# Optimization experiments

Hardware: AMD Instinct MI355X
Metric: run time of the kernel (lower is better)

Reference implementation:

```python
import jax, jax.numpy as jnp
import numpy as np

B, S, D = 4, 4096, 256


def setup_inputs() -> dict:
    key = jax.random.key(0)
    ks = jax.random.split(key, 12)
    s = 0.05
    return {
        "v": jax.random.normal(ks[0], (B, S, D), jnp.float32),
        "k": jax.random.normal(ks[1], (B, S, D), jnp.float32),
        "q": jax.random.normal(ks[2], (B, S, D), jnp.float32),
        "mask": jax.random.uniform(ks[3], (B, S, S), jnp.float32),
        "wq_k": jax.random.normal(ks[4], (D, D), jnp.float32) * s,
        "wq_b": jnp.zeros((D,), jnp.float32),
        "wk_k": jax.random.normal(ks[5], (D, D), jnp.float32) * s,
        "wk_b": jnp.zeros((D,), jnp.float32),
        "wv_k": jax.random.normal(ks[6], (D, D), jnp.float32) * s,
        "wv_b": jnp.zeros((D,), jnp.float32),
        "anchor": jax.random.normal(ks[7], (S, D), jnp.float32) * s,
        "dense_k": jax.random.normal(ks[8], (D, D), jnp.float32) * s,
        "dense_b": jnp.zeros((D,), jnp.float32),
    }


def reference(v, k, q, mask, wq_k, wq_b, wk_k, wk_b, wv_k, wv_b, anchor, dense_k, dense_b):
    # Bipolar linear projections
    qp = q @ wq_k + wq_b  # [B,Sq,D]
    kp = k @ wk_k + wk_b  # [B,Sk,D]
    vp = v @ wv_k + wv_b  # [B,Sk,D]

    # else-branch (Sq != D): k_ext = sign(k)[:,:,None,:] + sign(q)[:,None,:,:]
    # logits[b,i,j] = sum_d (sign(k)+sign(q))*sign(q)
    #              = sign(k)@sign(q)^T + sum_d sign(q)^2  (exact factorization)
    sq = jnp.sign(qp)
    sk = jnp.sign(kp)
    logits = (jnp.einsum('bkd,bqd->bkq', sk, sq)
              + jnp.sum(sq * sq, axis=-1)[:, None, :]) / 1024.0  # [B,Sk,Sq]

    attn = jax.nn.softmax(logits, axis=-1)  # softmax over Sq
    attn = attn * mask                      # mask applied AFTER softmax

    # output = attn^T @ v : [B,Sq,D]
    out = jnp.einsum('bkq,bkd->bqd', attn, vp)
    out = jnp.tanh(out * anchor)            # anchor broadcast [Sq,D]

    out = out @ dense_k + dense_b           # final Dense
    return out, attn
```

## Files before the change

kernel.cpp:

```cpp
#include <hip/hip_runtime.h>
#include <hip/hip_bf16.h>
#include <stdint.h>

#define NB 4
#define SS 4096
#define DD 256

typedef __attribute__((ext_vector_type(8))) short bf16x8;
typedef __attribute__((ext_vector_type(4))) float f32x4;

__device__ __forceinline__ float bf2f(uint16_t u) {
    union { uint32_t i; float f; } v; v.i = ((uint32_t)u) << 16; return v.f;
}
__device__ __forceinline__ uint16_t f2bf(float f) {
    union { float ff; uint32_t i; } v; v.ff = f;
    uint32_t r = v.i + 0x7FFFu + ((v.i >> 16) & 1u);
    return (uint16_t)(r >> 16);
}

__device__ __forceinline__ void gload_lds16(const uint16_t* g, uint16_t* l) {
    __builtin_amdgcn_global_load_lds((const __attribute__((address_space(1))) void*)g,
                                     (__attribute__((address_space(3))) void*)l, 16, 0, 0);
}

__global__ __launch_bounds__(256) void cast_f32_bf16(const float* __restrict__ in,
                                                     uint16_t* __restrict__ out, long n) {
    long i = ((long)blockIdx.x * 256 + threadIdx.x) * 8;
    if (i + 8 > n) return;
    float4 a = *(const float4*)(in + i);
    float4 b = *(const float4*)(in + i + 4);
    uint32_t w0 = (uint32_t)f2bf(a.x) | ((uint32_t)f2bf(a.y) << 16);
    uint32_t w1 = (uint32_t)f2bf(a.z) | ((uint32_t)f2bf(a.w) << 16);
    uint32_t w2 = (uint32_t)f2bf(b.x) | ((uint32_t)f2bf(b.y) << 16);
    uint32_t w3 = (uint32_t)f2bf(b.z) | ((uint32_t)f2bf(b.w) << 16);
    uint4 o; o.x = w0; o.y = w1; o.z = w2; o.w = w3;
    *(uint4*)(out + i) = o;
}

__global__ __launch_bounds__(256) void transpose_cast_w(const float* __restrict__ in,
                                                        uint16_t* __restrict__ out) {
    int t = blockIdx.x * 256 + threadIdx.x;
    int n = t >> 8, k = t & 255;
    out[t] = f2bf(in[k * 256 + n]);
}

__global__ __launch_bounds__(256) void transpose_bf16(const uint16_t* __restrict__ in,
                                                      uint16_t* __restrict__ out,
                                                      int R, int C, long ibs, long obs) {
    __shared__ uint16_t T[64][65];
    int b = blockIdx.z;
    int c0 = blockIdx.x * 64, r0 = blockIdx.y * 64;
    int t = threadIdx.x; int x = t & 63, y4 = t >> 6;
    const uint16_t* ib = in + (long)b * ibs;
    uint16_t* ob = out + (long)b * obs;
#pragma unroll
    for (int i = 0; i < 16; i++) {
        int rl = y4 + i * 4;
        T[rl][x] = ib[(long)(r0 + rl) * C + c0 + x];
    }
    __syncthreads();
#pragma unroll
    for (int i = 0; i < 16; i++) {
        int cc = y4 + i * 4;
        ob[(long)(c0 + cc) * R + r0 + x] = T[x][cc];
    }
}

__global__ __launch_bounds__(256) void attn_softmax_tr(const uint16_t* __restrict__ dots,
                                                       const float* __restrict__ mask,
                                                       const float* __restrict__ rowsum,
                                                       float* __restrict__ attn_out,
                                                       uint16_t* __restrict__ attnT) {
    __shared__ float T[64][65];
    int b = blockIdx.z;
    int q0 = blockIdx.x * 64, k0 = blockIdx.y * 64;
    int t = threadIdx.x; int x = t & 63, y4 = t >> 6;
    long base = (long)b * SS * SS;
#pragma unroll
    for (int i = 0; i < 16; i++) {
        int kl = y4 + i * 4;
        int kk = k0 + kl;
        long idx = base + (long)kk * SS + q0 + x;
        float d = bf2f(dots[idx]);
        float e = __expf(d * (1.0f / 1024.0f));
        float a = e * (1.0f / rowsum[b * SS + kk]) * mask[idx];
        attn_out[idx] = a;
        T[kl][x] = a;
    }
    __syncthreads();
#pragma unroll
    for (int i = 0; i < 16; i++) {
        int qq = y4 + i * 4;
        attnT[base + (long)(q0 + qq) * SS + k0 + x] = f2bf(T[x][qq]);
    }
}

template <int EPI>
__global__ __launch_bounds__(256) void gemm_bt(const uint16_t* __restrict__ A,
                                               const uint16_t* __restrict__ Bt,
                                               int M, int N, int K,
                                               long Abs, long Bbs, long Cbs,
                                               const float* __restrict__ bias,
                                               const float* __restrict__ anchor,
                                               float* __restrict__ rowsum,
                                               uint16_t* __restrict__ Cb,
                                               float* __restrict__ Cf) {
    __shared__ __align__(16) uint16_t As[128 * 32];
    __shared__ __align__(16) uint16_t Bs[128 * 32];
    const int t = threadIdx.x;
    const int l = t & 63;
    const int wid = t >> 6;
    const int wm = wid & 1, wn = wid >> 1;
    const int bz = blockIdx.z;
    const int m0 = blockIdx.y * 128;
    const int n0 = blockIdx.x * 128;

    const uint16_t* Ab = A + (long)bz * Abs + (long)m0 * K;
    const uint16_t* Bb = Bt + (long)bz * Bbs + (long)n0 * K;
    const uint16_t* ga = Ab + (long)(t >> 2) * K + (t & 3) * 8;
    const uint16_t* gb = Bb + (long)(t >> 2) * K + (t & 3) * 8;
    const long halfS = (long)64 * K;
    uint16_t* lA0 = As + (wid * 64) * 8;
    uint16_t* lA1 = As + (wid * 64) * 8 + 2048;
    uint16_t* lB0 = Bs + (wid * 64) * 8;
    uint16_t* lB1 = Bs + (wid * 64) * 8 + 2048;

    f32x4 acc[4][4];
#pragma unroll
    for (int i = 0; i < 4; i++)
#pragma unroll
        for (int j = 0; j < 4; j++) acc[i][j] = (f32x4){0.f, 0.f, 0.f, 0.f};

    const int aoff = (wm * 64 + (l & 15)) * 32 + (l >> 4) * 8;
    const int boff = (wn * 64 + (l & 15)) * 32 + (l >> 4) * 8;

    for (int kt = 0; kt < K; kt += 32) {
        if (kt) __syncthreads();
        gload_lds16(ga + kt, lA0);
        gload_lds16(ga + halfS + kt, lA1);
        gload_lds16(gb + kt, lB0);
        gload_lds16(gb + halfS + kt, lB1);
        __syncthreads();
        bf16x8 af[4], bfv[4];
#pragma unroll
        for (int i = 0; i < 4; i++) af[i] = *(const bf16x8*)(As + aoff + i * 512);
#pragma unroll
        for (int i = 0; i < 4; i++) bfv[i] = *(const bf16x8*)(Bs + boff + i * 512);
#pragma unroll
        for (int i = 0; i < 4; i++)
#pragma unroll
            for (int j = 0; j < 4; j++)
                acc[i][j] = __builtin_amdgcn_mfma_f32_16x16x32_bf16(af[i], bfv[j], acc[i][j], 0, 0, 0);
    }

    const int mb = m0 + wm * 64;
    const int nb = n0 + wn * 64;
    const int rl = (l >> 4) * 4;
    const int cl = l & 15;
    const long cbase = (long)bz * Cbs;

#pragma unroll
    for (int i = 0; i < 4; i++) {
#pragma unroll
        for (int r = 0; r < 4; r++) {
            const int mg = mb + i * 16 + rl + r;
            if constexpr (EPI == 0) {
                float s = 0.f;
#pragma unroll
                for (int j = 0; j < 4; j++) {
                    const int ng = nb + j * 16 + cl;
                    float vv = acc[i][j][r];
                    Cb[cbase + (long)mg * N + ng] = f2bf(vv);
                    s += __expf(vv * (1.0f / 1024.0f));
                }
                s += __shfl_xor(s, 1); s += __shfl_xor(s, 2);
                s += __shfl_xor(s, 4); s += __shfl_xor(s, 8);
                if (cl == 0) atomicAdd(&rowsum[(long)bz * M + mg], s);
            } else {
#pragma unroll
                for (int j = 0; j < 4; j++) {
                    const int ng = nb + j * 16 + cl;
                    float vv = acc[i][j][r];
                    if constexpr (EPI == 1) {
                        vv += bias[ng];
                        Cb[cbase + (long)mg * N + ng] =
                            (vv > 0.f) ? (uint16_t)0x3F80 : ((vv < 0.f) ? (uint16_t)0xBF80 : (uint16_t)0);
                    } else if constexpr (EPI == 2) {
                        Cb[cbase + (long)mg * N + ng] = f2bf(vv + bias[ng]);
                    } else if constexpr (EPI == 3) {
                        Cb[cbase + (long)mg * N + ng] = f2bf(tanhf(vv * anchor[(long)mg * N + ng]));
                    } else {
                        Cf[cbase + (long)mg * N + ng] = vv + bias[ng];
                    }
                }
            }
        }
    }
}

extern "C" void kernel_launch(void* const* d_in, const int* in_sizes, int n_in,
                              void* d_out, int out_size, void* d_ws, size_t ws_size,
                              hipStream_t stream) {
    const float* v_in   = (const float*)d_in[0];
    const float* k_in   = (const float*)d_in[1];
    const float* q_in   = (const float*)d_in[2];
    const float* mask   = (const float*)d_in[3];
    const float* wq_k   = (const float*)d_in[4];
    const float* wq_b   = (const float*)d_in[5];
    const float* wk_k   = (const float*)d_in[6];
    const float* wk_b   = (const float*)d_in[7];
    const float* wv_k   = (const float*)d_in[8];
    const float* wv_b   = (const float*)d_in[9];
    const float* anchor = (const float*)d_in[10];
    const float* dns_k  = (const float*)d_in[11];
    const float* dns_b  = (const float*)d_in[12];

    const long BSD = (long)NB * SS * DD;
    const long BSS = (long)NB * SS * SS;
    float* out0 = (float*)d_out;
    float* attn_out = out0 + BSD;

    char* w = (char*)d_ws;
    auto take = [&](long bytes) -> char* { char* p = w; w += (bytes + 255) & ~255L; return p; };
    uint16_t* qb   = (uint16_t*)take(BSD * 2);
    uint16_t* kb   = (uint16_t*)take(BSD * 2);
    uint16_t* vb   = (uint16_t*)take(BSD * 2);
    uint16_t* WTq  = (uint16_t*)take(65536L * 2);
    uint16_t* WTk  = (uint16_t*)take(65536L * 2);
    uint16_t* WTv  = (uint16_t*)take(65536L * 2);
    uint16_t* DT   = (uint16_t*)take(65536L * 2);
    uint16_t* sq   = (uint16_t*)take(BSD * 2);
    uint16_t* sk   = (uint16_t*)take(BSD * 2);
    uint16_t* vp   = (uint16_t*)take(BSD * 2);
    uint16_t* vpT  = (uint16_t*)take(BSD * 2);
    uint16_t* A2   = (uint16_t*)take(BSD * 2);
    uint16_t* dots = (uint16_t*)take(BSS * 2);
    uint16_t* attnT= (uint16_t*)take(BSS * 2);
    float* rowsum  = (float*)take((long)NB * SS * 4);

    cast_f32_bf16<<<dim3(BSD / 2048), 256, 0, stream>>>(q_in, qb, BSD);
    cast_f32_bf16<<<dim3(BSD / 2048), 256, 0, stream>>>(k_in, kb, BSD);
    cast_f32_bf16<<<dim3(BSD / 2048), 256, 0, stream>>>(v_in, vb, BSD);
    transpose_cast_w<<<256, 256, 0, stream>>>(wq_k, WTq);
    transpose_cast_w<<<256, 256, 0, stream>>>(wk_k, WTk);
    transpose_cast_w<<<256, 256, 0, stream>>>(wv_k, WTv);
    transpose_cast_w<<<256, 256, 0, stream>>>(dns_k, DT);
    hipMemsetAsync(rowsum, 0, (size_t)NB * SS * 4, stream);

    gemm_bt<1><<<dim3(2, 128, 1), 256, 0, stream>>>(qb, WTq, 16384, 256, 256, 0, 0, 0,
                                                    wq_b, nullptr, nullptr, sq, nullptr);
    gemm_bt<1><<<dim3(2, 128, 1), 256, 0, stream>>>(kb, WTk, 16384, 256, 256, 0, 0, 0,
                                                    wk_b, nullptr, nullptr, sk, nullptr);
    gemm_bt<2><<<dim3(2, 128, 1), 256, 0, stream>>>(vb, WTv, 16384, 256, 256, 0, 0, 0,
                                                    wv_b, nullptr, nullptr, vp, nullptr);
    transpose_bf16<<<dim3(4, 64, NB), 256, 0, stream>>>(vp, vpT, SS, DD,
                                                        (long)SS * DD, (long)SS * DD);

    gemm_bt<0><<<dim3(32, 32, NB), 256, 0, stream>>>(sk, sq, SS, SS, DD,
                                                     (long)SS * DD, (long)SS * DD, (long)SS * SS,
                                                     nullptr, nullptr, rowsum, dots, nullptr);

    attn_softmax_tr<<<dim3(64, 64, NB), 256, 0, stream>>>(dots, mask, rowsum, attn_out, attnT);

    gemm_bt<3><<<dim3(2, 32, NB), 256, 0, stream>>>(attnT, vpT, SS, DD, SS,
                                                    (long)SS * SS, (long)SS * DD, (long)SS * DD,
                                                    nullptr, anchor, nullptr, A2, nullptr);

    gemm_bt<4><<<dim3(2, 128, 1), 256, 0, stream>>>(A2, DT, 16384, 256, 256, 0, 0, 0,
                                                    dns_b, nullptr, nullptr, nullptr, out0);
}
```

Measured before the change: 801.3 us.

## Fuse logits recompute, softmax, mask and PV matmul into one attention kernel

The first GEMM now only computes row-wise exp sums, so the bf16 dots matrix is no longer written. A new fused kernel recomputes the sign(k)·sign(q) logits per 32-key tile, applies exp, normalisation and mask, writes attn, and feeds the probabilities through LDS straight into the PV MFMA with the tanh-anchor epilogue. This removes the large bf16 dots and transposed-attn round trips and two launches, at the cost of doing the QK matmul twice and leaving only 256 blocks of 512 threads with a sync-heavy inner loop. The four weight transpose-casts are also merged into one launch.

```diff
diff --git a/kernel.cpp b/kernel.cpp
--- a/kernel.cpp
+++ b/kernel.cpp
@@ -29,16 +29,25 @@
     if (i + 8 > n) return;
     float4 a = *(const float4*)(in + i);
     float4 b = *(const float4*)(in + i + 4);
-    uint32_t w0 = (uint32_t)f2bf(a.x) | ((uint32_t)f2bf(a.y) << 16);
-    uint32_t w1 = (uint32_t)f2bf(a.z) | ((uint32_t)f2bf(a.w) << 16);
-    uint32_t w2 = (uint32_t)f2bf(b.x) | ((uint32_t)f2bf(b.y) << 16);
-    uint32_t w3 = (uint32_t)f2bf(b.z) | ((uint32_t)f2bf(b.w) << 16);
-    uint4 o; o.x = w0; o.y = w1; o.z = w2; o.w = w3;
+    uint4 o;
+    o.x = (uint32_t)f2bf(a.x) | ((uint32_t)f2bf(a.y) << 16);
+    o.y = (uint32_t)f2bf(a.z) | ((uint32_t)f2bf(a.w) << 16);
+    o.z = (uint32_t)f2bf(b.x) | ((uint32_t)f2bf(b.y) << 16);
+    o.w = (uint32_t)f2bf(b.z) | ((uint32_t)f2bf(b.w) << 16);
     *(uint4*)(out + i) = o;
 }
 
-__global__ __launch_bounds__(256) void transpose_cast_w(const float* __restrict__ in,
-                                                        uint16_t* __restrict__ out) {
+__global__ __launch_bounds__(256) void transpose_cast_w4(const float* __restrict__ a0, const float* __restrict__ a1,
+                                                         const float* __restrict__ a2, const float* __restrict__ a3,
+                                                         uint16_t* __restrict__ o0, uint16_t* __restrict__ o1,
+                                                         uint16_t* __restrict__ o2, uint16_t* __restrict__ o3) {
+    const float* in; uint16_t* out;
+    switch (blockIdx.y) {
+        case 0: in = a0; out = o0; break;
+        case 1: in = a1; out = o1; break;
+        case 2: in = a2; out = o2; break;
+        default: in = a3; out = o3; break;
+    }
     int t = blockIdx.x * 256 + threadIdx.x;
     int n = t >> 8, k = t & 255;
     out[t] = f2bf(in[k * 256 + n]);
@@ -66,42 +75,12 @@
     }
 }
 
-__global__ __launch_bounds__(256) void attn_softmax_tr(const uint16_t* __restrict__ dots,
-                                                       const float* __restrict__ mask,
-                                                       const float* __restrict__ rowsum,
-                                                       float* __restrict__ attn_out,
-                                                       uint16_t* __restrict__ attnT) {
-    __shared__ float T[64][65];
-    int b = blockIdx.z;
-    int q0 = blockIdx.x * 64, k0 = blockIdx.y * 64;
-    int t = threadIdx.x; int x = t & 63, y4 = t >> 6;
-    long base = (long)b * SS * SS;
-#pragma unroll
-    for (int i = 0; i < 16; i++) {
-        int kl = y4 + i * 4;
-        int kk = k0 + kl;
-        long idx = base + (long)kk * SS + q0 + x;
-        float d = bf2f(dots[idx]);
-        float e = __expf(d * (1.0f / 1024.0f));
-        float a = e * (1.0f / rowsum[b * SS + kk]) * mask[idx];
-        attn_out[idx] = a;
-        T[kl][x] = a;
-    }
-    __syncthreads();
-#pragma unroll
-    for (int i = 0; i < 16; i++) {
-        int qq = y4 + i * 4;
-        attnT[base + (long)(q0 + qq) * SS + k0 + x] = f2bf(T[x][qq]);
-    }
-}
-
 template <int EPI>
 __global__ __launch_bounds__(256) void gemm_bt(const uint16_t* __restrict__ A,
                                                const uint16_t* __restrict__ Bt,
                                                int M, int N, int K,
                                                long Abs, long Bbs, long Cbs,
                                                const float* __restrict__ bias,
-                                               const float* __restrict__ anchor,
                                                float* __restrict__ rowsum,
                                                uint16_t* __restrict__ Cb,
                                                float* __restrict__ Cf) {
@@ -164,15 +143,10 @@
 #pragma unroll
         for (int r = 0; r < 4; r++) {
             const int mg = mb + i * 16 + rl + r;
-            if constexpr (EPI == 0) {
+            if constexpr (EPI == 5) {
                 float s = 0.f;
 #pragma unroll
-                for (int j = 0; j < 4; j++) {
-                    const int ng = nb + j * 16 + cl;
-                    float vv = acc[i][j][r];
-                    Cb[cbase + (long)mg * N + ng] = f2bf(vv);
-                    s += __expf(vv * (1.0f / 1024.0f));
-                }
+                for (int j = 0; j < 4; j++) s += __expf(acc[i][j][r] * (1.0f / 1024.0f));
                 s += __shfl_xor(s, 1); s += __shfl_xor(s, 2);
                 s += __shfl_xor(s, 4); s += __shfl_xor(s, 8);
                 if (cl == 0) atomicAdd(&rowsum[(long)bz * M + mg], s);
@@ -187,12 +161,126 @@
                             (vv > 0.f) ? (uint16_t)0x3F80 : ((vv < 0.f) ? (uint16_t)0xBF80 : (uint16_t)0);
                     } else if constexpr (EPI == 2) {
                         Cb[cbase + (long)mg * N + ng] = f2bf(vv + bias[ng]);
-                    } else if constexpr (EPI == 3) {
-                        Cb[cbase + (long)mg * N + ng] = f2bf(tanhf(vv * anchor[(long)mg * N + ng]));
                     } else {
                         Cf[cbase + (long)mg * N + ng] = vv + bias[ng];
                     }
                 }
+            }
+        }
+    }
+}
+
+__global__ __launch_bounds__(512, 2) void fused_attn_pv(const uint16_t* __restrict__ sk,
+                                                        const uint16_t* __restrict__ sq,
+                                                        const uint16_t* __restrict__ vpT,
+                                                        const float* __restrict__ mask,
+                                                        const float* __restrict__ rowsum,
+                                                        const float* __restrict__ anchor,
+                                                        float* __restrict__ attn_out,
+                                                        uint16_t* __restrict__ A2) {
+    __shared__ __align__(16) uint16_t Ks[2 * 8192];
+    __shared__ __align__(16) uint16_t Ts[64 * 40];
+
+    const int t = threadIdx.x;
+    const int w = t >> 6;
+    const int l = t & 63;
+    const int quad = l >> 4;
+    const int l15 = l & 15;
+    const int kh = w & 1;
+    const int qq = w >> 2 == 0 ? (w >> 1) : (w >> 1);
+    const int qql = w >> 1;
+    const int dsl = w * 32;
+
+    const int b = blockIdx.y;
+    const int q0 = blockIdx.x * 64;
+
+    const uint16_t* sqb = sq + (long)b * SS * DD;
+    const uint16_t* skb = sk + (long)b * SS * DD;
+    const uint16_t* vtb = vpT + (long)b * SS * DD;
+    const float* maskb = mask + (long)b * SS * SS;
+    float* attnb = attn_out + (long)b * SS * SS;
+    const float* rsb = rowsum + (long)b * SS;
+
+    bf16x8 qf[8];
+#pragma unroll
+    for (int s = 0; s < 8; s++)
+        qf[s] = *(const bf16x8*)(sqb + (long)(q0 + qql * 16 + l15) * DD + s * 32 + quad * 8);
+
+    f32x4 acc[4][2];
+#pragma unroll
+    for (int i = 0; i < 4; i++) { acc[i][0] = (f32x4){0,0,0,0}; acc[i][1] = (f32x4){0,0,0,0}; }
+
+    const uint16_t* gK = skb + (long)(l >> 2) * DD + w * 32 + (l & 3) * 8;
+
+    {
+        uint16_t* base = Ks + w * 1024;
+        gload_lds16(gK, base);
+        gload_lds16(gK + 16 * DD, base + 512);
+    }
+
+    const int NIT = SS / 32;
+    for (int it = 0; it < NIT; ++it) {
+        const int kt = it * 32;
+        __syncthreads();
+
+        if (it + 1 < NIT) {
+            uint16_t* base = Ks + ((it + 1) & 1) * 8192 + w * 1024;
+            const uint16_t* g = gK + (long)(kt + 32) * DD;
+            gload_lds16(g, base);
+            gload_lds16(g + 16 * DD, base + 512);
+        }
+
+        bf16x8 vf0 = *(const bf16x8*)(vtb + (long)(dsl + l15) * SS + kt + quad * 8);
+        bf16x8 vf1 = *(const bf16x8*)(vtb + (long)(dsl + 16 + l15) * SS + kt + quad * 8);
+        const int kg0 = kt + kh * 16 + quad * 4;
+        float mr[4], inv[4];
+#pragma unroll
+        for (int r = 0; r < 4; r++) mr[r] = maskb[(long)(kg0 + r) * SS + q0 + qql * 16 + l15];
+#pragma unroll
+        for (int r = 0; r < 4; r++) inv[r] = __builtin_amdgcn_rcpf(rsb[kg0 + r]);
+
+        f32x4 lacc = (f32x4){0, 0, 0, 0};
+        const uint16_t* kbuf = Ks + (it & 1) * 8192;
+#pragma unroll
+        for (int s = 0; s < 8; s++) {
+            bf16x8 kf = *(const bf16x8*)(kbuf + s * 1024 + (kh * 16 + l15) * 32 + quad * 8);
+            lacc = __builtin_amdgcn_mfma_f32_16x16x32_bf16(kf, qf[s], lacc, 0, 0, 0);
+        }
+
+        float av[4];
+#pragma unroll
+        for (int r = 0; r < 4; r++) {
+            float e = __expf(lacc[r] * (1.0f / 1024.0f));
+            float a = e * inv[r] * mr[r];
+            attnb[(long)(kg0 + r) * SS + q0 + qql * 16 + l15] = a;
+            av[r] = a;
+        }
+        uint2 pk;
+        pk.x = (uint32_t)f2bf(av[0]) | ((uint32_t)f2bf(av[1]) << 16);
+        pk.y = (uint32_t)f2bf(av[2]) | ((uint32_t)f2bf(av[3]) << 16);
+        *(uint2*)&Ts[(qql * 16 + l15) * 40 + kh * 16 + quad * 4] = pk;
+
+        __syncthreads();
+
+#pragma unroll
+        for (int qi = 0; qi < 4; qi++) {
+            bf16x8 tf = *(const bf16x8*)(Ts + (qi * 16 + l15) * 40 + quad * 8);
+            acc[qi][0] = __builtin_amdgcn_mfma_f32_16x16x32_bf16(tf, vf0, acc[qi][0], 0, 0, 0);
+            acc[qi][1] = __builtin_amdgcn_mfma_f32_16x16x32_bf16(tf, vf1, acc[qi][1], 0, 0, 0);
+        }
+    }
+
+    uint16_t* A2b = A2 + (long)b * SS * DD;
+#pragma unroll
+    for (int qi = 0; qi < 4; qi++) {
+#pragma unroll
+        for (int dj = 0; dj < 2; dj++) {
+#pragma unroll
+            for (int r = 0; r < 4; r++) {
+                const int q = q0 + qi * 16 + quad * 4 + r;
+                const int d = dsl + dj * 16 + l15;
+                float o = acc[qi][dj][r];
+                A2b[(long)q * DD + d] = f2bf(tanhf(o * anchor[(long)q * DD + d]));
             }
         }
     }
@@ -216,7 +304,6 @@
     const float* dns_b  = (const float*)d_in[12];
 
     const long BSD = (long)NB * SS * DD;
-    const long BSS = (long)NB * SS * SS;
     float* out0 = (float*)d_out;
     float* attn_out = out0 + BSD;
 
@@ -234,38 +321,31 @@
     uint16_t* vp   = (uint16_t*)take(BSD * 2);
     uint16_t* vpT  = (uint16_t*)take(BSD * 2);
     uint16_t* A2   = (uint16_t*)take(BSD * 2);
-    uint16_t* dots = (uint16_t*)take(BSS * 2);
-    uint16_t* attnT= (uint16_t*)take(BSS * 2);
     float* rowsum  = (float*)take((long)NB * SS * 4);
+
+    hipMemsetAsync(rowsum, 0, (size_t)NB * SS * 4, stream);
 
     cast_f32_bf16<<<dim3(BSD / 2048), 256, 0, stream>>>(q_in, qb, BSD);
     cast_f32_bf16<<<dim3(BSD / 2048), 256, 0, stream>>>(k_in, kb, BSD);
     cast_f32_bf16<<<dim3(BSD / 2048), 256, 0, stream>>>(v_in, vb, BSD);
-    transpose_cast_w<<<256, 256, 0, stream>>>(wq_k, WTq);
-    transpose_cast_w<<<256, 256, 0, stream>>>(wk_k, WTk);
-    transpose_cast_w<<<256, 256, 0, stream>>>(wv_k, WTv);
-    transpose_cast_w<<<256, 256, 0, stream>>>(dns_k, DT);
-    hipMemsetAsync(rowsum, 0, (size_t)NB * SS * 4, stream);
+    transpose_cast_w4<<<dim3(256, 4), 256, 0, stream>>>(wq_k, wk_k, wv_k, dns_k, WTq, WTk, WTv, DT);
 
     gemm_bt<1><<<dim3(2, 128, 1), 256, 0, stream>>>(qb, WTq, 16384, 256, 256, 0, 0, 0,
-                                                    wq_b, nullptr, nullptr, sq, nullptr);
+                                                    wq_b, nullptr, sq, nullptr);
     gemm_bt<1><<<dim3(2, 128, 1), 256, 0, stream>>>(kb, WTk, 16384, 256, 256, 0, 0, 0,
-                                                    wk_b, nullptr, nullptr, sk, nullptr);
+                                                    wk_b, nullptr, sk, nullptr);
     gemm_bt<2><<<dim3(2, 128, 1), 256, 0, stream>>>(vb, WTv, 16384, 256, 256, 0, 0, 0,
-                                                    wv_b, nullptr, nullptr, vp, nullptr);
+                                                    wv_b, nullptr, vp, nullptr);
     transpose_bf16<<<dim3(4, 64, NB), 256, 0, stream>>>(vp, vpT, SS, DD,
                                                         (long)SS * DD, (long)SS * DD);
 
-    gemm_bt<0><<<dim3(32, 32, NB), 256, 0, stream>>>(sk, sq, SS, SS, DD,
-                                                     (long)SS * DD, (long)SS * DD, (long)SS * SS,
-                                                     nullptr, nullptr, rowsum, dots, nullptr);
-
-    attn_softmax_tr<<<dim3(64, 64, NB), 256, 0, stream>>>(dots, mask, rowsum, attn_out, attnT);
-
-    gemm_bt<3><<<dim3(2, 32, NB), 256, 0, stream>>>(attnT, vpT, SS, DD, SS,
-                                                    (long)SS * SS, (long)SS * DD, (long)SS * DD,
-                                                    nullptr, anchor, nullptr, A2, nullptr);
+    gemm_bt<5><<<dim3(32, 32, NB), 256, 0, stream>>>(sk, sq, SS, SS, DD,
+                                                     (long)SS * DD, (long)SS * DD, 0,
+                                                     nullptr, rowsum, nullptr, nullptr);
+
+    fused_attn_pv<<<dim3(SS / 64, NB), 512, 0, stream>>>(sk, sq, vpT, mask, rowsum,
+                                                         anchor, attn_out, A2);
 
     gemm_bt<4><<<dim3(2, 128, 1), 256, 0, stream>>>(A2, DT, 16384, 256, 256, 0, 0, 0,
-                                                    dns_b, nullptr, nullptr, nullptr, out0);
-}
+                                                    dns_b, nullptr, nullptr, out0);
+}
```

Measured after the change: 779.2 us. 2.8% less time.
